# Performance work log

Hardware: AMD Instinct MI355X
Metric: run time of the kernel (lower is better)

The kernel has to match this reference:

```python
import jax, jax.numpy as jnp
import numpy as np

B, T, E, H, D = 256, 77, 1280, 20, 64
SCALE = D ** -0.5
NEG = -1e9


def setup_inputs() -> dict:
    key = jax.random.key(0)
    ks = jax.random.split(key, 32)
    w = lambda k, shape, s=0.02: jax.random.normal(k, shape, dtype=jnp.float32) * s
    causal = jnp.triu(jnp.full((T, T), NEG, dtype=jnp.float32), k=1)
    causal_mask = jnp.broadcast_to(causal[None, None], (B, 1, T, T))
    return {
        'hidden_states': jax.random.normal(ks[0], (B, T, E), dtype=jnp.float32),
        'embeds': jax.random.normal(ks[1], (B, T, E), dtype=jnp.float32),
        'causal_mask': causal_mask,
        'q_w': w(ks[2], (E, E)), 'q_b': w(ks[3], (E,)),
        'k_w': w(ks[4], (E, E)), 'k_b': w(ks[5], (E,)),
        'v_w': w(ks[6], (E, E)), 'v_b': w(ks[7], (E,)),
        'o_w': w(ks[8], (E, E)), 'o_b': w(ks[9], (E,)),
        'ka_w': w(ks[10], (E, E)) * 0.01, 'ka_b': w(ks[11], (E,)) * 0.001,
        'va_w': w(ks[12], (E, E)) * 0.01, 'va_b': w(ks[13], (E,)) * 0.001,
        'zc1_w': w(ks[14], (E, E)), 'zc1_b': w(ks[15], (E,)),
        'zt1_w': w(ks[16], (T, 2 * T)), 'zt1_b': w(ks[17], (T,)),
        'zc2_w': w(ks[18], (E, E)), 'zc2_b': w(ks[19], (E,)),
        'zt2_w': w(ks[20], (T, T)), 'zt2_b': w(ks[21], (T,)),
    }


def _heads(x):
    # (B, S, E) -> (B, H, S, D)
    return x.reshape(B, -1, H, D).transpose(0, 2, 1, 3)


def _attend(q, k, v, mask=None):
    # q,k,v: (B,H,*,D); returns (B,T,E)
    logits = jnp.einsum('bhtd,bhsd->bhts', q, k)
    if mask is not None:
        logits = logits + mask  # mask: (B,1,T,S)
    probs = jax.nn.softmax(logits, axis=-1)  # dropout p=0 in eval
    ctx = jnp.einsum('bhts,bhsd->bhtd', probs, v)
    return ctx.transpose(0, 2, 1, 3).reshape(B, T, E)


def _zipper(x, zc1_w, zc1_b, zt1_w, zt1_b, zc2_w, zc2_b, zt2_w, zt2_b):
    # token/channel mixer: (B, 2T, E) -> (B, T, E)
    x = jax.nn.gelu(x @ zc1_w.T + zc1_b)              # channel: E -> hidden E
    x = jnp.swapaxes(x, 1, 2)                          # (B, E, 2T)
    x = jax.nn.gelu(x @ zt1_w.T + zt1_b)               # tokens: 2T -> T
    x = jnp.swapaxes(x, 1, 2)                          # (B, T, E)
    x = x @ zc2_w.T + zc2_b                            # channel: E -> E
    x = jnp.swapaxes(x, 1, 2) @ zt2_w.T + zt2_b        # tokens: T -> T
    return jnp.swapaxes(x, 1, 2)


def reference(hidden_states, embeds, causal_mask,
              q_w, q_b, k_w, k_b, v_w, v_b, o_w, o_b,
              ka_w, ka_b, va_w, va_b,
              zc1_w, zc1_b, zt1_w, zt1_b, zc2_w, zc2_b, zt2_w, zt2_b):
    q = _heads((hidden_states @ q_w.T + q_b) * SCALE)
    k = _heads(hidden_states @ k_w.T + k_b)
    v = _heads(hidden_states @ v_w.T + v_b)
    attn_output = _attend(q, k, v, causal_mask)  # self-attention pass

    # adapter cross-attention pass (shared query)
    ka = _heads(embeds @ ka_w.T + ka_b)
    va = _heads(embeds @ va_w.T + va_b)
    attn_output_adapter = _attend(q, ka, va, None)

    zipped = _zipper(jnp.concatenate([attn_output_adapter, attn_output], axis=1),
                     zc1_w, zc1_b, zt1_w, zt1_b, zc2_w, zc2_b, zt2_w, zt2_b)
    attn_output = attn_output + zipped
    return attn_output @ o_w.T + o_b
```

## Files before the change

### kernel.cpp

```cpp
#include <hip/hip_runtime.h>
#include <stdint.h>

#define B_    256
#define T_    77
#define E_    1280
#define H_    20
#define T2_   154
#define MTOK  19712
#define MTOK2 39424

typedef float f32x4 __attribute__((ext_vector_type(4)));
typedef short bf16x8 __attribute__((ext_vector_type(8)));

__device__ inline float bf2f(short s) {
    return __uint_as_float(((unsigned)(unsigned short)s) << 16);
}
__device__ inline short f2bf(float f) {
    unsigned u = __float_as_uint(f);
    u += 0x7fff + ((u >> 16) & 1);
    return (short)(u >> 16);
}
__device__ inline float gelu_tanh(float x) {
    float x3 = x * x * x;
    return 0.5f * x * (1.0f + tanhf(0.7978845608028654f * (x + 0.044715f * x3)));
}

__global__ void cast_f32_bf16(const float* __restrict__ in, short* __restrict__ out, int n4) {
    int i = blockIdx.x * blockDim.x + threadIdx.x;
    int stride = gridDim.x * blockDim.x;
    for (; i < n4; i += stride) {
        float4 v = reinterpret_cast<const float4*>(in)[i];
        short4 o;
        o.x = f2bf(v.x); o.y = f2bf(v.y); o.z = f2bf(v.z); o.w = f2bf(v.w);
        reinterpret_cast<short4*>(out)[i] = o;
    }
}

__global__ void pad_weight(const float* __restrict__ W, short* __restrict__ Wp,
                           int rows, int cols, int KP) {
    int i = blockIdx.x * 256 + threadIdx.x;
    if (i >= 80 * KP) return;
    int t = i / KP, s = i - t * KP;
    Wp[i] = (t < rows && s < cols) ? f2bf(W[t * cols + s]) : (short)0;
}

template<int EPI>
__global__ void gemm_bt(const short* __restrict__ A, const short* __restrict__ W,
                        const float* __restrict__ bias, void* __restrict__ Cout,
                        int K, float scale) {
    const int N = E_;
    const int NBN = E_ / 128;
    __shared__ short Als[128 * 64];
    __shared__ short Bls[128 * 64];
    const int tid  = threadIdx.x;
    const int wave = tid >> 6, lane = tid & 63;

    const int nwg = gridDim.x;
    const int qq = nwg >> 3, rr = nwg & 7;
    const int x = blockIdx.x & 7, ii = blockIdx.x >> 3;
    const int L = (x < rr ? x * (qq + 1) : rr * (qq + 1) + (x - rr) * qq) + ii;
    const int bm = L / NBN, bn = L % NBN;

    const int wm = (wave >> 1) * 64, wn = (wave & 1) * 64;

    f32x4 acc[4][4] = {};

    const long arow0 = (long)bm * 128;
    const long brow0 = (long)bn * 128;
    const int rsub = lane >> 3;
    const int col  = (lane & 7) * 8;

    for (int kt = 0; kt < K; kt += 64) {
        __syncthreads();
#pragma unroll
        for (int i = 0; i < 4; ++i) {
            int chunk = i * 4 + wave;
            int row = chunk * 8 + rsub;
            const short* ga = A + (arow0 + row) * K + kt + col;
            const short* gb = W + (brow0 + row) * K + kt + col;
            __builtin_amdgcn_global_load_lds(
                (const __attribute__((address_space(1))) unsigned int*)ga,
                (__attribute__((address_space(3))) unsigned int*)&Als[chunk * 512], 16, 0, 0);
            __builtin_amdgcn_global_load_lds(
                (const __attribute__((address_space(1))) unsigned int*)gb,
                (__attribute__((address_space(3))) unsigned int*)&Bls[chunk * 512], 16, 0, 0);
        }
        __syncthreads();
#pragma unroll
        for (int kk = 0; kk < 2; ++kk) {
            bf16x8 af[4], bfr[4];
#pragma unroll
            for (int mi = 0; mi < 4; ++mi)
                af[mi] = *reinterpret_cast<const bf16x8*>(
                    &Als[(wm + mi * 16 + (lane & 15)) * 64 + kk * 32 + (lane >> 4) * 8]);
#pragma unroll
            for (int nj = 0; nj < 4; ++nj)
                bfr[nj] = *reinterpret_cast<const bf16x8*>(
                    &Bls[(wn + nj * 16 + (lane & 15)) * 64 + kk * 32 + (lane >> 4) * 8]);
#pragma unroll
            for (int mi = 0; mi < 4; ++mi)
#pragma unroll
                for (int nj = 0; nj < 4; ++nj)
                    acc[mi][nj] = __builtin_amdgcn_mfma_f32_16x16x32_bf16(
                        af[mi], bfr[nj], acc[mi][nj], 0, 0, 0);
        }
    }

#pragma unroll
    for (int mi = 0; mi < 4; ++mi) {
#pragma unroll
        for (int nj = 0; nj < 4; ++nj) {
            int gcol = bn * 128 + wn + nj * 16 + (lane & 15);
            float bv = bias[gcol];
#pragma unroll
            for (int r = 0; r < 4; ++r) {
                long grow = arow0 + wm + mi * 16 + (lane >> 4) * 4 + r;
                float v = acc[mi][nj][r] + bv;
                if (EPI == 1) v *= scale;
                if (EPI == 2) v = gelu_tanh(v);
                if (EPI == 3) ((float*)Cout)[grow * N + gcol] = v;
                else          ((short*)Cout)[grow * N + gcol] = f2bf(v);
            }
        }
    }
}

template<int SIN, int KP, int PS, bool GELU, bool RESID>
__global__ void mixer_mfma(const short* __restrict__ IN, const short* __restrict__ Wp,
                           const float* __restrict__ bias, const short* __restrict__ Cat,
                           short* __restrict__ OUT) {
    __shared__ short lsT[64 * PS];
    const int e0 = blockIdx.x * 64;
    const int b  = blockIdx.y;
    const int tid = threadIdx.x, wave = tid >> 6, lane = tid & 63;

    const int eg = tid & 7;
    const int sl = tid >> 3;
    for (int sb = sl; sb < KP; sb += 32) {
        if (sb < SIN) {
            bf16x8 v = *reinterpret_cast<const bf16x8*>(
                &IN[((long)b * SIN + sb) * E_ + e0 + eg * 8]);
#pragma unroll
            for (int i = 0; i < 8; ++i)
                lsT[(eg * 8 + i) * PS + sb] = v[i];
        } else {
#pragma unroll
            for (int i = 0; i < 8; ++i)
                lsT[(eg * 8 + i) * PS + sb] = 0;
        }
    }
    __syncthreads();

    const int ebase = wave * 16;
    f32x4 acc[5] = {};
#pragma unroll
    for (int ks = 0; ks < KP / 32; ++ks) {
        bf16x8 bfr = *reinterpret_cast<const bf16x8*>(
            &lsT[(ebase + (lane & 15)) * PS + ks * 32 + (lane >> 4) * 8]);
#pragma unroll
        for (int mt = 0; mt < 5; ++mt) {
            bf16x8 af = *reinterpret_cast<const bf16x8*>(
                &Wp[(mt * 16 + (lane & 15)) * KP + ks * 32 + (lane >> 4) * 8]);
            acc[mt] = __builtin_amdgcn_mfma_f32_16x16x32_bf16(af, bfr, acc[mt], 0, 0, 0);
        }
    }

    const int e = e0 + ebase + (lane & 15);
#pragma unroll
    for (int mt = 0; mt < 5; ++mt) {
#pragma unroll
        for (int r = 0; r < 4; ++r) {
            int t = mt * 16 + (lane >> 4) * 4 + r;
            if (t < T_) {
                float v = acc[mt][r] + bias[t];
                if (GELU) v = gelu_tanh(v);
                if (RESID) v += bf2f(Cat[((long)b * T2_ + T_ + t) * E_ + e]);
                OUT[((long)b * T_ + t) * E_ + e] = f2bf(v);
            }
        }
    }
}

#define ASTR 104
__global__ __launch_bounds__(64, 1)
void attn_mfma(const short* __restrict__ Qm,
               const short* __restrict__ Km, const short* __restrict__ Vm,
               const short* __restrict__ KAm, const short* __restrict__ VAm,
               short* __restrict__ Cat) {
    __shared__ short pls[80 * ASTR];
    __shared__ short vt[64 * ASTR];
    const int hh = blockIdx.x;
    const int b = hh / H_, h = hh % H_;
    const int lane = threadIdx.x & 63;
    const int colbase = lane & 15, g = lane >> 4;
    const long base = ((long)b * T_) * E_ + h * 64;

    for (int pass = 0; pass < 2; ++pass) {
        const short* Kp = pass ? KAm : Km;
        const short* Vp = pass ? VAm : Vm;
        const bool causal = (pass == 0);
        const int rowoff = pass ? 0 : T_;

        {
            int4 z = {0, 0, 0, 0};
#pragma unroll
            for (int it = 0; it < 4; ++it) {
                int idx = it * 64 + lane;
                int row = idx >> 2, cb = idx & 3;
                *reinterpret_cast<int4*>(&vt[row * ASTR + 64 + cb * 8]) = z;
            }
#pragma unroll
            for (int it = 0; it < 3; ++it) {
                int idx = it * 64 + lane;
                if (idx < 160) {
                    int row = idx >> 1, cb = idx & 1;
                    *reinterpret_cast<int4*>(&pls[row * ASTR + 80 + cb * 8]) = z;
                }
            }
        }

        {
            const short* vb = Vp + base + (long)lane * E_;
#pragma unroll
            for (int dg = 0; dg < 8; ++dg) {
                bf16x8 v = *reinterpret_cast<const bf16x8*>(vb + dg * 8);
#pragma unroll
                for (int i = 0; i < 8; ++i) vt[(dg * 8 + i) * ASTR + lane] = v[i];
            }
            if (lane < T_ - 64) {
                const short* vb2 = Vp + base + (long)(64 + lane) * E_;
#pragma unroll
                for (int dg = 0; dg < 8; ++dg) {
                    bf16x8 v = *reinterpret_cast<const bf16x8*>(vb2 + dg * 8);
#pragma unroll
                    for (int i = 0; i < 8; ++i) vt[(dg * 8 + i) * ASTR + 64 + lane] = v[i];
                }
            }
        }

        f32x4 sacc[5][5] = {};
#pragma unroll
        for (int kk = 0; kk < 2; ++kk) {
            bf16x8 qf[5];
#pragma unroll
            for (int mi = 0; mi < 5; ++mi) {
                int t = mi * 16 + colbase; t = t > 76 ? 76 : t;
                qf[mi] = *reinterpret_cast<const bf16x8*>(
                    Qm + base + (long)t * E_ + kk * 32 + g * 8);
            }
#pragma unroll
            for (int nj = 0; nj < 5; ++nj) {
                int s = nj * 16 + colbase; s = s > 76 ? 76 : s;
                bf16x8 kf = *reinterpret_cast<const bf16x8*>(
                    Kp + base + (long)s * E_ + kk * 32 + g * 8);
#pragma unroll
                for (int mi = 0; mi < 5; ++mi)
                    sacc[mi][nj] = __builtin_amdgcn_mfma_f32_16x16x32_bf16(
                        qf[mi], kf, sacc[mi][nj], 0, 0, 0);
            }
        }

        float inv[5][4];
#pragma unroll
        for (int mi = 0; mi < 5; ++mi) {
#pragma unroll
            for (int r = 0; r < 4; ++r) {
                int t = mi * 16 + g * 4 + r;
                float mx = -3.0e38f;
#pragma unroll
                for (int nj = 0; nj < 5; ++nj) {
                    int s = nj * 16 + colbase;
                    bool ok = causal ? (s <= t) : (s < T_);
                    if (ok) mx = fmaxf(mx, sacc[mi][nj][r]);
                }
#pragma unroll
                for (int o = 1; o <= 8; o <<= 1) mx = fmaxf(mx, __shfl_xor(mx, o));
                float sum = 0.f;
#pragma unroll
                for (int nj = 0; nj < 5; ++nj) {
                    int s = nj * 16 + colbase;
                    bool ok = causal ? (s <= t) : (s < T_);
                    float pv = ok ? __expf(sacc[mi][nj][r] - mx) : 0.f;
                    sacc[mi][nj][r] = pv;
                    sum += pv;
                }
#pragma unroll
                for (int o = 1; o <= 8; o <<= 1) sum += __shfl_xor(sum, o);
                inv[mi][r] = 1.0f / sum;
            }
        }

#pragma unroll
        for (int mi = 0; mi < 5; ++mi)
#pragma unroll
            for (int nj = 0; nj < 5; ++nj)
#pragma unroll
                for (int r = 0; r < 4; ++r)
                    pls[(mi * 16 + g * 4 + r) * ASTR + nj * 16 + colbase] =
                        f2bf(sacc[mi][nj][r]);

        f32x4 cacc[5][4] = {};
#pragma unroll
        for (int ks = 0; ks < 3; ++ks) {
            bf16x8 pa[5];
#pragma unroll
            for (int mi = 0; mi < 5; ++mi)
                pa[mi] = *reinterpret_cast<const bf16x8*>(
                    &pls[(mi * 16 + colbase) * ASTR + ks * 32 + g * 8]);
#pragma unroll
            for (int nd = 0; nd < 4; ++nd) {
                bf16x8 vf = *reinterpret_cast<const bf16x8*>(
                    &vt[(nd * 16 + colbase) * ASTR + ks * 32 + g * 8]);
#pragma unroll
                for (int mi = 0; mi < 5; ++mi)
                    cacc[mi][nd] = __builtin_amdgcn_mfma_f32_16x16x32_bf16(
                        pa[mi], vf, cacc[mi][nd], 0, 0, 0);
            }
        }

#pragma unroll
        for (int mi = 0; mi < 5; ++mi)
#pragma unroll
            for (int nd = 0; nd < 4; ++nd)
#pragma unroll
                for (int r = 0; r < 4; ++r) {
                    int t = mi * 16 + g * 4 + r;
                    if (t < T_) {
                        float val = cacc[mi][nd][r] * inv[mi][r];
                        Cat[((long)b * T2_ + rowoff + t) * E_ + h * 64 + nd * 16 + colbase] =
                            f2bf(val);
                    }
                }
    }
}

extern "C" void kernel_launch(void* const* d_in, const int* in_sizes, int n_in,
                              void* d_out, int out_size, void* d_ws, size_t ws_size,
                              hipStream_t stream) {
    const float* hidden = (const float*)d_in[0];
    const float* embeds = (const float*)d_in[1];
    const float* q_w  = (const float*)d_in[3];  const float* q_b  = (const float*)d_in[4];
    const float* k_w  = (const float*)d_in[5];  const float* k_b  = (const float*)d_in[6];
    const float* v_w  = (const float*)d_in[7];  const float* v_b  = (const float*)d_in[8];
    const float* o_w  = (const float*)d_in[9];  const float* o_b  = (const float*)d_in[10];
    const float* ka_w = (const float*)d_in[11]; const float* ka_b = (const float*)d_in[12];
    const float* va_w = (const float*)d_in[13]; const float* va_b = (const float*)d_in[14];
    const float* zc1_w = (const float*)d_in[15]; const float* zc1_b = (const float*)d_in[16];
    const float* zt1_w = (const float*)d_in[17]; const float* zt1_b = (const float*)d_in[18];
    const float* zc2_w = (const float*)d_in[19]; const float* zc2_b = (const float*)d_in[20];
    const float* zt2_w = (const float*)d_in[21]; const float* zt2_b = (const float*)d_in[22];

    char* ws = (char*)d_ws;
    const size_t WSZ = (size_t)E_ * E_ * 2;
    const size_t ASZ = (size_t)MTOK * E_ * 2;
    short* Wq  = (short*)(ws + 0 * WSZ);
    short* Wk  = (short*)(ws + 1 * WSZ);
    short* Wv  = (short*)(ws + 2 * WSZ);
    short* Wka = (short*)(ws + 3 * WSZ);
    short* Wva = (short*)(ws + 4 * WSZ);
    short* Wz1 = (short*)(ws + 5 * WSZ);
    short* Wz2 = (short*)(ws + 6 * WSZ);
    short* Wo  = (short*)(ws + 7 * WSZ);
    char* p = ws + 8 * WSZ;
    short* Ahs  = (short*)p; p += ASZ;
    short* Aemb = (short*)p; p += ASZ;
    short* Qb   = (short*)p; p += ASZ;
    short* Kb   = (short*)p; p += ASZ;
    short* Vb   = (short*)p; p += ASZ;
    short* KAb  = (short*)p; p += ASZ;
    short* VAb  = (short*)p; p += ASZ;
    short* Wz1p = (short*)p; p += 80 * 160 * 2;
    short* Wz2p = (short*)p; p += 80 * 96 * 2;
    short* CAT = Ahs;
    short* Y   = KAb;
    short* X2  = Qb;
    short* X3  = Kb;
    short* S   = Vb;

    if (ws_size < (size_t)(p - ws)) return;

    cast_f32_bf16<<<2048, 256, 0, stream>>>(hidden, Ahs,  MTOK * E_ / 4);
    cast_f32_bf16<<<2048, 256, 0, stream>>>(embeds, Aemb, MTOK * E_ / 4);
    cast_f32_bf16<<<512, 256, 0, stream>>>(q_w,  Wq,  E_ * E_ / 4);
    cast_f32_bf16<<<512, 256, 0, stream>>>(k_w,  Wk,  E_ * E_ / 4);
    cast_f32_bf16<<<512, 256, 0, stream>>>(v_w,  Wv,  E_ * E_ / 4);
    cast_f32_bf16<<<512, 256, 0, stream>>>(ka_w, Wka, E_ * E_ / 4);
    cast_f32_bf16<<<512, 256, 0, stream>>>(va_w, Wva, E_ * E_ / 4);
    cast_f32_bf16<<<512, 256, 0, stream>>>(zc1_w, Wz1, E_ * E_ / 4);
    cast_f32_bf16<<<512, 256, 0, stream>>>(zc2_w, Wz2, E_ * E_ / 4);
    cast_f32_bf16<<<512, 256, 0, stream>>>(o_w,  Wo,  E_ * E_ / 4);
    pad_weight<<<(80 * 160 + 255) / 256, 256, 0, stream>>>(zt1_w, Wz1p, 77, 154, 160);
    pad_weight<<<(80 * 96 + 255) / 256, 256, 0, stream>>>(zt2_w, Wz2p, 77, 77, 96);

    const int g154 = (MTOK / 128) * (E_ / 128);
    const int g308 = (MTOK2 / 128) * (E_ / 128);
    gemm_bt<1><<<g154, 256, 0, stream>>>(Ahs,  Wq,  q_b,  Qb,  E_, 0.125f);
    gemm_bt<0><<<g154, 256, 0, stream>>>(Ahs,  Wk,  k_b,  Kb,  E_, 1.f);
    gemm_bt<0><<<g154, 256, 0, stream>>>(Ahs,  Wv,  v_b,  Vb,  E_, 1.f);
    gemm_bt<0><<<g154, 256, 0, stream>>>(Aemb, Wka, ka_b, KAb, E_, 1.f);
    gemm_bt<0><<<g154, 256, 0, stream>>>(Aemb, Wva, va_b, VAb, E_, 1.f);
    attn_mfma<<<B_ * H_, 64, 0, stream>>>(Qb, Kb, Vb, KAb, VAb, CAT);
    gemm_bt<2><<<g308, 256, 0, stream>>>(CAT, Wz1, zc1_b, Y, E_, 1.f);
    mixer_mfma<154, 160, 168, true, false><<<dim3(E_ / 64, B_), 256, 0, stream>>>(
        Y, Wz1p, zt1_b, nullptr, X2);
    gemm_bt<0><<<g154, 256, 0, stream>>>(X2, Wz2, zc2_b, X3, E_, 1.f);
    mixer_mfma<77, 96, 104, false, true><<<dim3(E_ / 64, B_), 256, 0, stream>>>(
        X3, Wz2p, zt2_b, CAT, S);
    gemm_bt<3><<<g154, 256, 0, stream>>>(S, Wo, o_b, (float*)d_out, E_, 1.f);
}
```

Before: 1.129 ms.

## Fuse QKV and adapter KV projections into wide GEMMs and swizzle LDS tiles

Replaces the five separate projection GEMMs with two wider launches. One computes Q, K and V together, the other computes the adapter K and V, and each output segment picks its own bias, scale and destination in the epilogue. This cuts launch count and gives larger grids. Separately, the shared GEMM core now loads A and B tiles into LDS with an XOR swizzle on 16-byte columns and reads them with the matching swizzle, to reduce LDS bank conflicts on the fragment reads. The fused projections assume the Q/K/V and KA/VA bf16 weight buffers sit contiguously in the workspace.

```diff
diff --git a/kernel.cpp b/kernel.cpp
--- a/kernel.cpp
+++ b/kernel.cpp
@@ -44,10 +44,54 @@
     Wp[i] = (t < rows && s < cols) ? f2bf(W[t * cols + s]) : (short)0;
 }
 
+#define GEMM_CORE(A_, W_, KDIM, ACC)                                                   \
+    const int rsub = lane >> 3;                                                        \
+    const int col  = (((lane & 7) ^ rsub) & 7) * 8;                                    \
+    const int swz  = (lane & 7) << 3;                                                  \
+    for (int kt = 0; kt < (KDIM); kt += 64) {                                          \
+        __syncthreads();                                                               \
+        _Pragma("unroll")                                                              \
+        for (int i = 0; i < 4; ++i) {                                                  \
+            int chunk = i * 4 + wave;                                                  \
+            int row = chunk * 8 + rsub;                                                \
+            const short* ga = (A_) + (arow0 + row) * (KDIM) + kt + col;                \
+            const short* gb = (W_) + (brow0 + row) * (KDIM) + kt + col;                \
+            __builtin_amdgcn_global_load_lds(                                          \
+                (const __attribute__((address_space(1))) unsigned int*)ga,             \
+                (__attribute__((address_space(3))) unsigned int*)&Als[chunk * 512],    \
+                16, 0, 0);                                                             \
+            __builtin_amdgcn_global_load_lds(                                          \
+                (const __attribute__((address_space(1))) unsigned int*)gb,             \
+                (__attribute__((address_space(3))) unsigned int*)&Bls[chunk * 512],    \
+                16, 0, 0);                                                             \
+        }                                                                              \
+        __syncthreads();                                                               \
+        _Pragma("unroll")                                                              \
+        for (int kk = 0; kk < 2; ++kk) {                                               \
+            bf16x8 af[4], bfr[4];                                                      \
+            _Pragma("unroll")                                                          \
+            for (int mi = 0; mi < 4; ++mi)                                             \
+                af[mi] = *reinterpret_cast<const bf16x8*>(                             \
+                    &Als[(((wm + mi * 16 + (lane & 15)) * 64 + kk * 32 +               \
+                           (lane >> 4) * 8)) ^ swz]);                                  \
+            _Pragma("unroll")                                                          \
+            for (int nj = 0; nj < 4; ++nj)                                             \
+                bfr[nj] = *reinterpret_cast<const bf16x8*>(                            \
+                    &Bls[(((wn + nj * 16 + (lane & 15)) * 64 + kk * 32 +               \
+                           (lane >> 4) * 8)) ^ swz]);                                  \
+            _Pragma("unroll")                                                          \
+            for (int mi = 0; mi < 4; ++mi)                                             \
+                _Pragma("unroll")                                                      \
+                for (int nj = 0; nj < 4; ++nj)                                         \
+                    ACC[mi][nj] = __builtin_amdgcn_mfma_f32_16x16x32_bf16(             \
+                        af[mi], bfr[nj], ACC[mi][nj], 0, 0, 0);                        \
+        }                                                                              \
+    }
+
 template<int EPI>
 __global__ void gemm_bt(const short* __restrict__ A, const short* __restrict__ W,
                         const float* __restrict__ bias, void* __restrict__ Cout,
-                        int K, float scale) {
+                        int K) {
     const int N = E_;
     const int NBN = E_ / 128;
     __shared__ short Als[128 * 64];
@@ -62,49 +106,11 @@
     const int bm = L / NBN, bn = L % NBN;
 
     const int wm = (wave >> 1) * 64, wn = (wave & 1) * 64;
-
     f32x4 acc[4][4] = {};
-
     const long arow0 = (long)bm * 128;
     const long brow0 = (long)bn * 128;
-    const int rsub = lane >> 3;
-    const int col  = (lane & 7) * 8;
-
-    for (int kt = 0; kt < K; kt += 64) {
-        __syncthreads();
-#pragma unroll
-        for (int i = 0; i < 4; ++i) {
-            int chunk = i * 4 + wave;
-            int row = chunk * 8 + rsub;
-            const short* ga = A + (arow0 + row) * K + kt + col;
-            const short* gb = W + (brow0 + row) * K + kt + col;
-            __builtin_amdgcn_global_load_lds(
-                (const __attribute__((address_space(1))) unsigned int*)ga,
-                (__attribute__((address_space(3))) unsigned int*)&Als[chunk * 512], 16, 0, 0);
-            __builtin_amdgcn_global_load_lds(
-                (const __attribute__((address_space(1))) unsigned int*)gb,
-                (__attribute__((address_space(3))) unsigned int*)&Bls[chunk * 512], 16, 0, 0);
-        }
-        __syncthreads();
-#pragma unroll
-        for (int kk = 0; kk < 2; ++kk) {
-            bf16x8 af[4], bfr[4];
-#pragma unroll
-            for (int mi = 0; mi < 4; ++mi)
-                af[mi] = *reinterpret_cast<const bf16x8*>(
-                    &Als[(wm + mi * 16 + (lane & 15)) * 64 + kk * 32 + (lane >> 4) * 8]);
-#pragma unroll
-            for (int nj = 0; nj < 4; ++nj)
-                bfr[nj] = *reinterpret_cast<const bf16x8*>(
-                    &Bls[(wn + nj * 16 + (lane & 15)) * 64 + kk * 32 + (lane >> 4) * 8]);
-#pragma unroll
-            for (int mi = 0; mi < 4; ++mi)
-#pragma unroll
-                for (int nj = 0; nj < 4; ++nj)
-                    acc[mi][nj] = __builtin_amdgcn_mfma_f32_16x16x32_bf16(
-                        af[mi], bfr[nj], acc[mi][nj], 0, 0, 0);
-        }
-    }
+
+    GEMM_CORE(A, W, K, acc)
 
 #pragma unroll
     for (int mi = 0; mi < 4; ++mi) {
@@ -116,10 +122,55 @@
             for (int r = 0; r < 4; ++r) {
                 long grow = arow0 + wm + mi * 16 + (lane >> 4) * 4 + r;
                 float v = acc[mi][nj][r] + bv;
-                if (EPI == 1) v *= scale;
                 if (EPI == 2) v = gelu_tanh(v);
                 if (EPI == 3) ((float*)Cout)[grow * N + gcol] = v;
                 else          ((short*)Cout)[grow * N + gcol] = f2bf(v);
+            }
+        }
+    }
+}
+
+template<int NSEG>
+__global__ void gemm_proj(const short* __restrict__ A, const short* __restrict__ W,
+                          const float* __restrict__ b0, const float* __restrict__ b1,
+                          const float* __restrict__ b2,
+                          short* __restrict__ o0, short* __restrict__ o1,
+                          short* __restrict__ o2, float s0) {
+    const int NBN = NSEG * (E_ / 128);
+    __shared__ short Als[128 * 64];
+    __shared__ short Bls[128 * 64];
+    const int tid  = threadIdx.x;
+    const int wave = tid >> 6, lane = tid & 63;
+
+    const int nwg = gridDim.x;
+    const int qq = nwg >> 3, rr = nwg & 7;
+    const int x = blockIdx.x & 7, ii = blockIdx.x >> 3;
+    const int L = (x < rr ? x * (qq + 1) : rr * (qq + 1) + (x - rr) * qq) + ii;
+    const int bm = L / NBN, bn = L % NBN;
+
+    const int wm = (wave >> 1) * 64, wn = (wave & 1) * 64;
+    f32x4 acc[4][4] = {};
+    const long arow0 = (long)bm * 128;
+    const long brow0 = (long)bn * 128;
+    const int K = E_;
+
+    GEMM_CORE(A, W, K, acc)
+
+    const int seg = bn / (E_ / 128);
+    const float* bias = seg == 0 ? b0 : (seg == 1 ? b1 : b2);
+    short* out = seg == 0 ? o0 : (seg == 1 ? o1 : o2);
+    const float scl = seg == 0 ? s0 : 1.f;
+    const int bnl = bn - seg * (E_ / 128);
+#pragma unroll
+    for (int mi = 0; mi < 4; ++mi) {
+#pragma unroll
+        for (int nj = 0; nj < 4; ++nj) {
+            int gcol = bnl * 128 + wn + nj * 16 + (lane & 15);
+            float bv = bias[gcol];
+#pragma unroll
+            for (int r = 0; r < 4; ++r) {
+                long grow = arow0 + wm + mi * 16 + (lane >> 4) * 4 + r;
+                out[grow * E_ + gcol] = f2bf((acc[mi][nj][r] + bv) * scl);
             }
         }
     }
@@ -392,19 +443,20 @@
     pad_weight<<<(80 * 160 + 255) / 256, 256, 0, stream>>>(zt1_w, Wz1p, 77, 154, 160);
     pad_weight<<<(80 * 96 + 255) / 256, 256, 0, stream>>>(zt2_w, Wz2p, 77, 77, 96);
 
-    const int g154 = (MTOK / 128) * (E_ / 128);
-    const int g308 = (MTOK2 / 128) * (E_ / 128);
-    gemm_bt<1><<<g154, 256, 0, stream>>>(Ahs,  Wq,  q_b,  Qb,  E_, 0.125f);
-    gemm_bt<0><<<g154, 256, 0, stream>>>(Ahs,  Wk,  k_b,  Kb,  E_, 1.f);
-    gemm_bt<0><<<g154, 256, 0, stream>>>(Ahs,  Wv,  v_b,  Vb,  E_, 1.f);
-    gemm_bt<0><<<g154, 256, 0, stream>>>(Aemb, Wka, ka_b, KAb, E_, 1.f);
-    gemm_bt<0><<<g154, 256, 0, stream>>>(Aemb, Wva, va_b, VAb, E_, 1.f);
+    const int gQKV  = (MTOK / 128) * (3 * E_ / 128);
+    const int gKAVA = (MTOK / 128) * (2 * E_ / 128);
+    const int g154  = (MTOK / 128) * (E_ / 128);
+    const int g308  = (MTOK2 / 128) * (E_ / 128);
+    gemm_proj<3><<<gQKV, 256, 0, stream>>>(Ahs, Wq, q_b, k_b, v_b,
+                                           Qb, Kb, Vb, 0.125f);
+    gemm_proj<2><<<gKAVA, 256, 0, stream>>>(Aemb, Wka, ka_b, va_b, nullptr,
+                                            KAb, VAb, nullptr, 1.f);
     attn_mfma<<<B_ * H_, 64, 0, stream>>>(Qb, Kb, Vb, KAb, VAb, CAT);
-    gemm_bt<2><<<g308, 256, 0, stream>>>(CAT, Wz1, zc1_b, Y, E_, 1.f);
+    gemm_bt<2><<<g308, 256, 0, stream>>>(CAT, Wz1, zc1_b, Y, E_);
     mixer_mfma<154, 160, 168, true, false><<<dim3(E_ / 64, B_), 256, 0, stream>>>(
         Y, Wz1p, zt1_b, nullptr, X2);
-    gemm_bt<0><<<g154, 256, 0, stream>>>(X2, Wz2, zc2_b, X3, E_, 1.f);
+    gemm_bt<0><<<g154, 256, 0, stream>>>(X2, Wz2, zc2_b, X3, E_);
     mixer_mfma<77, 96, 104, false, true><<<dim3(E_ / 64, B_), 256, 0, stream>>>(
         X3, Wz2p, zt2_b, CAT, S);
-    gemm_bt<3><<<g154, 256, 0, stream>>>(S, Wo, o_b, (float*)d_out, E_, 1.f);
-}
+    gemm_bt<3><<<g154, 256, 0, stream>>>(S, Wo, o_b, (float*)d_out, E_);
+}
```

Measured after the change: 1.099 ms. 2.7% less time.
